# Kernel optimization log

Measured on AMD Instinct MI355X. Metric: run time of the kernel, lower is better.

Reference implementation:

```python
import jax, jax.numpy as jnp
import numpy as np

N = 100000
E = 1600000
IN_C, HID_C, OUT_C, NUM_CLASSES = 128, 64, 64, 40


def glorot(key, shape):
    lim = float(np.sqrt(6.0 / (shape[0] + shape[1])))
    return jax.random.uniform(key, shape, jnp.float32, -lim, lim)


def setup_inputs() -> dict:
    key = jax.random.key(0)
    ks = jax.random.split(key, 8)
    x = jax.random.normal(ks[0], (N, IN_C), jnp.float32)
    edge_index = jax.random.randint(ks[1], (2, E), 0, N, jnp.int64)
    return {
        "x": x,
        "edge_index": edge_index,
        "W1": glorot(ks[2], (IN_C, HID_C)),
        "b1": jnp.zeros((HID_C,), jnp.float32),
        "W2": glorot(ks[3], (HID_C, OUT_C)),
        "b2": jnp.zeros((OUT_C,), jnp.float32),
        "Wf": glorot(ks[4], (OUT_C, NUM_CLASSES)),
        "bf": jnp.zeros((NUM_CLASSES,), jnp.float32),
    }


def gcn_conv(x, W, b, src, dst, n):
    # PyG GCNConv: out = D^{-1/2} (A + I) D^{-1/2} (x W) + b, self-loops added.
    h = x @ W  # [N, C_out]
    loop = jnp.arange(n, dtype=src.dtype)
    src_f = jnp.concatenate([src, loop])  # [E+N]
    dst_f = jnp.concatenate([dst, loop])
    deg = jax.ops.segment_sum(jnp.ones_like(dst_f, dtype=h.dtype), dst_f,
                              num_segments=n)  # in-degree incl. self-loop
    inv_sqrt = jnp.where(deg > 0, jax.lax.rsqrt(deg), 0.0)
    norm = inv_sqrt[src_f] * inv_sqrt[dst_f]  # [E+N]
    msg = h[src_f] * norm[:, None]  # gather + scale, [E+N, C_out]
    out = jax.ops.segment_sum(msg, dst_f, num_segments=n)  # scatter-add
    return out + b


def reference(x, edge_index, W1, b1, W2, b2, Wf, bf):
    src, dst = edge_index[0], edge_index[1]
    n = x.shape[0]
    h = jax.nn.relu(gcn_conv(x, W1, b1, src, dst, n))
    h = jax.nn.relu(gcn_conv(h, W2, b2, src, dst, n))
    return h @ Wf + bf
```

## Files before the change

kernel.cpp:

```cpp
#include <hip/hip_runtime.h>

constexpr int N_NODES = 100000;
constexpr int N_EDGES = 1600000;
constexpr int IN_C  = 128;
constexpr int HID_C = 64;
constexpr int NUM_CLASSES = 40;

constexpr int BSH = 9;
constexpr int BUCK_N = 1 << BSH;
constexpr int NBUCK = (N_NODES + BUCK_N - 1) >> BSH;
constexpr int BCAP = 9216;
constexpr int FS_EPT = 16;
constexpr int FS_T = 256;
constexpr int FS_CHUNK = FS_EPT * FS_T;
constexpr int FS_BLKS = (N_EDGES + FS_CHUNK - 1) / FS_CHUNK;

typedef __attribute__((ext_vector_type(8))) short bf16x8;
typedef __attribute__((ext_vector_type(4))) short short4v;
typedef __attribute__((ext_vector_type(4))) float f32x4;

__device__ __forceinline__ unsigned short f2bf(float f) {
    unsigned u = __float_as_uint(f);
    return (unsigned short)((u + 0x7FFFu + ((u >> 16) & 1u)) >> 16);
}
__device__ __forceinline__ float bf2f(unsigned short h) {
    return __uint_as_float((unsigned)h << 16);
}

__global__ __launch_bounds__(FS_T) void fill_stage_kernel(
        const int* __restrict__ src, const int* __restrict__ dst,
        unsigned* __restrict__ gcur, unsigned* __restrict__ stage) {
    __shared__ unsigned hist[NBUCK];
    __shared__ unsigned rbase[NBUCK];
    int t = threadIdx.x;
    for (int i = t; i < NBUCK; i += FS_T) hist[i] = 0u;
    __syncthreads();
    int e0 = blockIdx.x * FS_CHUNK + t;
    unsigned pay[FS_EPT];
    unsigned br[FS_EPT];
#pragma unroll
    for (int i = 0; i < FS_EPT; ++i) {
        int e = e0 + i * FS_T;
        br[i] = 0xFFFFFFFFu; pay[i] = 0u;
        if (e < N_EDGES) {
            unsigned d = (unsigned)dst[e];
            unsigned s = (unsigned)src[e];
            unsigned b = d >> BSH;
            unsigned r = atomicAdd(&hist[b], 1u);
            pay[i] = (s << BSH) | (d & (BUCK_N - 1u));
            br[i]  = (b << 16) | r;
        }
    }
    __syncthreads();
    for (int i = t; i < NBUCK; i += FS_T) {
        unsigned c = hist[i];
        rbase[i] = c ? ((unsigned)i * BCAP + atomicAdd(&gcur[i], c)) : 0u;
    }
    __syncthreads();
#pragma unroll
    for (int i = 0; i < FS_EPT; ++i) {
        if (br[i] != 0xFFFFFFFFu) {
            unsigned bb = br[i] >> 16;
            unsigned idx = rbase[bb] + (br[i] & 0xFFFFu);
            if (idx < (bb + 1u) * BCAP) stage[idx] = pay[i];
        }
    }
}

__global__ __launch_bounds__(512) void fill_final_kernel(
        const unsigned* __restrict__ gcur,
        const unsigned* __restrict__ stage, unsigned* __restrict__ rowptr,
        float* __restrict__ inv, unsigned* __restrict__ csr_src) {
    __shared__ unsigned cur[BUCK_N];
    __shared__ unsigned ps[512];
    __shared__ unsigned buf[BCAP];
    int b = blockIdx.x, t = threadIdx.x;
    int lo = b << BSH;
    int nn = min(BUCK_N, N_NODES - lo);
    unsigned gv = (t < NBUCK) ? gcur[t] : 0u;
    ps[t] = gv;
    __syncthreads();
    for (int off = 1; off < 256; off <<= 1) {
        unsigned u = (t >= off) ? ps[t - off] : 0u;
        __syncthreads();
        ps[t] += u;
        __syncthreads();
    }
    unsigned base = ps[b] - gcur[b];
    if (b == NBUCK - 1 && t == 0) rowptr[N_NODES] = ps[NBUCK - 1];
    unsigned c = min(gcur[b], (unsigned)BCAP);
    const unsigned* st = stage + (size_t)b * BCAP;
    cur[t] = 0u;
    __syncthreads();
    for (int i = t; i < (int)c; i += 512) atomicAdd(&cur[st[i] & (BUCK_N - 1u)], 1u);
    __syncthreads();
    unsigned d = cur[t];
    ps[t] = d;
    __syncthreads();
    for (int off = 1; off < 512; off <<= 1) {
        unsigned u = (t >= off) ? ps[t - off] : 0u;
        __syncthreads();
        ps[t] += u;
        __syncthreads();
    }
    unsigned off0 = ps[t] - d;
    if (t < nn) {
        rowptr[lo + t] = base + off0;
        inv[lo + t] = rsqrtf((float)(d + 1u));
    }
    __syncthreads();
    cur[t] = off0;
    __syncthreads();
    for (int i = t; i < (int)c; i += 512) {
        unsigned v = st[i];
        unsigned pos = atomicAdd(&cur[v & (BUCK_N - 1u)], 1u);
        buf[pos] = v >> BSH;
    }
    __syncthreads();
    for (int i = t; i < (int)c; i += 512) csr_src[base + i] = buf[i];
}

template <int K, bool BF>
__global__ __launch_bounds__(256) void gemm_mfma_kernel(
        const void* __restrict__ Xv, const float* __restrict__ W,
        const float* __restrict__ inv, unsigned short* __restrict__ out, int n) {
    __shared__ __align__(16) short Asd[64][K + 8];
    __shared__ __align__(16) short Bsd[64][K + 8];
    int t = threadIdx.x;
    int n0 = blockIdx.x * 64;
    if (BF) {
        const uint4* Xb = (const uint4*)Xv;
        for (int i = t; i < 64 * (K / 8); i += 256) {
            int row = i / (K / 8), seg = i % (K / 8);
            int node = n0 + row;
            uint4 v = {0, 0, 0, 0};
            if (node < n) v = Xb[(size_t)node * (K / 8) + seg];
            *(uint4*)&Asd[row][seg * 8] = v;
        }
    } else {
        const float* Xf = (const float*)Xv;
        for (int i = t; i < 64 * (K / 4); i += 256) {
            int row = i / (K / 4), seg = i % (K / 4);
            int node = n0 + row;
            float4 v = {0, 0, 0, 0};
            if (node < n) v = *(const float4*)&Xf[(size_t)node * K + seg * 4];
            short4v o;
            o.x = (short)f2bf(v.x); o.y = (short)f2bf(v.y);
            o.z = (short)f2bf(v.z); o.w = (short)f2bf(v.w);
            *(short4v*)&Asd[row][seg * 4] = o;
        }
    }
    for (int i = t; i < K * 16; i += 256) {
        int k = i >> 4, ng = i & 15;
        float4 v = *(const float4*)&W[(size_t)k * 64 + ng * 4];
        Bsd[ng * 4 + 0][k] = (short)f2bf(v.x);
        Bsd[ng * 4 + 1][k] = (short)f2bf(v.y);
        Bsd[ng * 4 + 2][k] = (short)f2bf(v.z);
        Bsd[ng * 4 + 3][k] = (short)f2bf(v.w);
    }
    __syncthreads();
    int wv = t >> 6, lane = t & 63;
    int m = lane & 15, quad = lane >> 4;
    int rowbase = wv * 16;
    f32x4 acc0 = {0,0,0,0}, acc1 = {0,0,0,0}, acc2 = {0,0,0,0}, acc3 = {0,0,0,0};
#pragma unroll
    for (int kb = 0; kb < K / 32; ++kb) {
        bf16x8 af = *(const bf16x8*)&Asd[rowbase + m][kb * 32 + quad * 8];
        bf16x8 b0 = *(const bf16x8*)&Bsd[ 0 + m][kb * 32 + quad * 8];
        bf16x8 b1 = *(const bf16x8*)&Bsd[16 + m][kb * 32 + quad * 8];
        bf16x8 b2 = *(const bf16x8*)&Bsd[32 + m][kb * 32 + quad * 8];
        bf16x8 b3 = *(const bf16x8*)&Bsd[48 + m][kb * 32 + quad * 8];
        acc0 = __builtin_amdgcn_mfma_f32_16x16x32_bf16(af, b0, acc0, 0, 0, 0);
        acc1 = __builtin_amdgcn_mfma_f32_16x16x32_bf16(af, b1, acc1, 0, 0, 0);
        acc2 = __builtin_amdgcn_mfma_f32_16x16x32_bf16(af, b2, acc2, 0, 0, 0);
        acc3 = __builtin_amdgcn_mfma_f32_16x16x32_bf16(af, b3, acc3, 0, 0, 0);
    }
    f32x4 accs[4] = {acc0, acc1, acc2, acc3};
#pragma unroll
    for (int r = 0; r < 4; ++r) {
        int node = n0 + rowbase + quad * 4 + r;
        if (node < n) {
            float sc = inv[node];
#pragma unroll
            for (int s = 0; s < 4; ++s)
                out[(size_t)node * 64 + s * 16 + m] = f2bf(accs[s][r] * sc);
        }
    }
}

__global__ __launch_bounds__(256) void agg_fused_kernel(
        const unsigned* __restrict__ rowptr, const unsigned* __restrict__ csr_src,
        const unsigned short* __restrict__ hs, const float* __restrict__ inv,
        const float* __restrict__ bias, unsigned short* __restrict__ out) {
    int t = threadIdx.x;
    int lane = t & 63;
    int oct = lane >> 3;
    int cl  = lane & 7;
    int node = blockIdx.x * 32 + (t >> 6) * 8 + oct;
    unsigned beg = rowptr[node], end = rowptr[node + 1];
    float a0 = 0.f, a1 = 0.f, a2 = 0.f, a3 = 0.f;
    float a4 = 0.f, a5 = 0.f, a6 = 0.f, a7 = 0.f;
    const uint4* hsrow = (const uint4*)hs;
#pragma unroll 4
    for (unsigned e = beg; e < end; ++e) {
        unsigned s = csr_src[e];
        uint4 v = hsrow[(size_t)s * 8 + cl];
        a0 += __uint_as_float(v.x << 16);
        a1 += __uint_as_float(v.x & 0xFFFF0000u);
        a2 += __uint_as_float(v.y << 16);
        a3 += __uint_as_float(v.y & 0xFFFF0000u);
        a4 += __uint_as_float(v.z << 16);
        a5 += __uint_as_float(v.z & 0xFFFF0000u);
        a6 += __uint_as_float(v.w << 16);
        a7 += __uint_as_float(v.w & 0xFFFF0000u);
    }
    uint4 sv = hsrow[(size_t)node * 8 + cl];
    float4 bv0 = *(const float4*)&bias[cl * 8];
    float4 bv1 = *(const float4*)&bias[cl * 8 + 4];
    float s = inv[node];
    float r0 = fmaxf(s * (a0 + __uint_as_float(sv.x << 16))         + bv0.x, 0.f);
    float r1 = fmaxf(s * (a1 + __uint_as_float(sv.x & 0xFFFF0000u)) + bv0.y, 0.f);
    float r2 = fmaxf(s * (a2 + __uint_as_float(sv.y << 16))         + bv0.z, 0.f);
    float r3 = fmaxf(s * (a3 + __uint_as_float(sv.y & 0xFFFF0000u)) + bv0.w, 0.f);
    float r4 = fmaxf(s * (a4 + __uint_as_float(sv.z << 16))         + bv1.x, 0.f);
    float r5 = fmaxf(s * (a5 + __uint_as_float(sv.z & 0xFFFF0000u)) + bv1.y, 0.f);
    float r6 = fmaxf(s * (a6 + __uint_as_float(sv.w << 16))         + bv1.z, 0.f);
    float r7 = fmaxf(s * (a7 + __uint_as_float(sv.w & 0xFFFF0000u)) + bv1.w, 0.f);
    uint4 o;
    o.x = (unsigned)f2bf(r0) | ((unsigned)f2bf(r1) << 16);
    o.y = (unsigned)f2bf(r2) | ((unsigned)f2bf(r3) << 16);
    o.z = (unsigned)f2bf(r4) | ((unsigned)f2bf(r5) << 16);
    o.w = (unsigned)f2bf(r6) | ((unsigned)f2bf(r7) << 16);
    ((uint4*)out)[(size_t)node * 8 + cl] = o;
}

__global__ __launch_bounds__(320) void final_gemm_kernel(
        const unsigned short* __restrict__ H, const float* __restrict__ Wf,
        const float* __restrict__ bfv, float* __restrict__ out, int n) {
    constexpr int CK = 64, J = 40;
    __shared__ float Ws[CK * J];
    __shared__ float Hs[CK][132];
    int t = threadIdx.x;
    int n0 = blockIdx.x * 128;
    for (int i = t; i < CK * J / 4; i += 320)
        ((float4*)Ws)[i] = ((const float4*)Wf)[i];
    for (int i = t; i < 128 * 16; i += 320) {
        int row = i >> 4, kc = i & 15;
        int node = n0 + row;
        ushort4 v = {0, 0, 0, 0};
        if (node < n) v = *(const ushort4*)&H[(size_t)node * 64 + kc * 4];
        Hs[kc * 4 + 0][row] = bf2f(v.x);
        Hs[kc * 4 + 1][row] = bf2f(v.y);
        Hs[kc * 4 + 2][row] = bf2f(v.z);
        Hs[kc * 4 + 3][row] = bf2f(v.w);
    }
    __syncthreads();
    int cg = t % 10;
    int rg = t / 10;
    float4 a0 = {0,0,0,0}, a1 = {0,0,0,0}, a2 = {0,0,0,0}, a3 = {0,0,0,0};
#pragma unroll 8
    for (int k = 0; k < CK; ++k) {
        float4 b = *(const float4*)&Ws[k * J + cg * 4];
        float4 a = *(const float4*)&Hs[k][rg * 4];
        a0.x += a.x * b.x; a0.y += a.x * b.y; a0.z += a.x * b.z; a0.w += a.x * b.w;
        a1.x += a.y * b.x; a1.y += a.y * b.y; a1.z += a.y * b.z; a1.w += a.y * b.w;
        a2.x += a.z * b.x; a2.y += a.z * b.y; a2.z += a.z * b.z; a2.w += a.z * b.w;
        a3.x += a.w * b.x; a3.y += a.w * b.y; a3.z += a.w * b.z; a3.w += a.w * b.w;
    }
    float4 bv = *(const float4*)&bfv[cg * 4];
    float4 accs[4] = {a0, a1, a2, a3};
#pragma unroll
    for (int i = 0; i < 4; ++i) {
        int node = n0 + rg * 4 + i;
        if (node < n) {
            float4 r = accs[i];
            r.x += bv.x; r.y += bv.y; r.z += bv.z; r.w += bv.w;
            *(float4*)&out[(size_t)node * J + cg * 4] = r;
        }
    }
}

extern "C" void kernel_launch(void* const* d_in, const int* in_sizes, int n_in,
                              void* d_out, int out_size, void* d_ws, size_t ws_size,
                              hipStream_t stream) {
    const float* x  = (const float*)d_in[0];
    const int*   ei = (const int*)d_in[1];
    const float* W1 = (const float*)d_in[2];
    const float* b1 = (const float*)d_in[3];
    const float* W2 = (const float*)d_in[4];
    const float* b2 = (const float*)d_in[5];
    const float* Wf = (const float*)d_in[6];
    const float* bf = (const float*)d_in[7];
    float* out = (float*)d_out;

    const int* src = ei;
    const int* dst = ei + N_EDGES;

    char* ws = (char*)d_ws;
    unsigned* rowptr  = (unsigned*)(ws + 0);
    float*    inv     = (float*)   (ws + 400064);
    unsigned* gcur    = (unsigned*)(ws + 800064);
    unsigned* csr_src = (unsigned*)(ws + 801792);
    unsigned short* A = (unsigned short*)(ws + 7201792);
    unsigned short* B = (unsigned short*)(ws + 20001792);
    unsigned* stage   = (unsigned*)A;

    hipMemsetAsync(gcur, 0, NBUCK * sizeof(unsigned), stream);
    fill_stage_kernel<<<FS_BLKS, FS_T, 0, stream>>>(src, dst, gcur, stage);
    fill_final_kernel<<<NBUCK, 512, 0, stream>>>(gcur, stage, rowptr, inv, csr_src);

    gemm_mfma_kernel<IN_C, false>
        <<<(N_NODES + 63) / 64, 256, 0, stream>>>(x, W1, inv, A, N_NODES);
    agg_fused_kernel<<<N_NODES / 32, 256, 0, stream>>>(rowptr, csr_src, A, inv, b1, B);

    gemm_mfma_kernel<HID_C, true>
        <<<(N_NODES + 63) / 64, 256, 0, stream>>>(B, W2, inv, A, N_NODES);
    agg_fused_kernel<<<N_NODES / 32, 256, 0, stream>>>(rowptr, csr_src, A, inv, b2, B);

    final_gemm_kernel<<<(N_NODES + 127) / 128, 320, 0, stream>>>(B, Wf, bf, out, N_NODES);
}
```

Baseline: 244.8 us.

## Fuse aggregation with following GEMM to drop intermediate feature round-trips

Layer-1 aggregation is merged with the layer-2 MFMA GEMM, and layer-2 aggregation is merged with the final classifier GEMM. Each block aggregates 64 nodes into shared memory, then multiplies by the weights directly. This removes two kernel launches and the global write and re-read of the bf16 hidden activations. In exchange, the latency-bound gather phase now shares a block with GEMM work. The final GEMM also uses only 160 of 256 threads, which could lower occupancy or overlap.

```diff
diff --git a/kernel.cpp b/kernel.cpp
--- a/kernel.cpp
+++ b/kernel.cpp
@@ -120,87 +120,12 @@
     for (int i = t; i < (int)c; i += 512) csr_src[base + i] = buf[i];
 }
 
-template <int K, bool BF>
-__global__ __launch_bounds__(256) void gemm_mfma_kernel(
-        const void* __restrict__ Xv, const float* __restrict__ W,
-        const float* __restrict__ inv, unsigned short* __restrict__ out, int n) {
-    __shared__ __align__(16) short Asd[64][K + 8];
-    __shared__ __align__(16) short Bsd[64][K + 8];
-    int t = threadIdx.x;
-    int n0 = blockIdx.x * 64;
-    if (BF) {
-        const uint4* Xb = (const uint4*)Xv;
-        for (int i = t; i < 64 * (K / 8); i += 256) {
-            int row = i / (K / 8), seg = i % (K / 8);
-            int node = n0 + row;
-            uint4 v = {0, 0, 0, 0};
-            if (node < n) v = Xb[(size_t)node * (K / 8) + seg];
-            *(uint4*)&Asd[row][seg * 8] = v;
-        }
-    } else {
-        const float* Xf = (const float*)Xv;
-        for (int i = t; i < 64 * (K / 4); i += 256) {
-            int row = i / (K / 4), seg = i % (K / 4);
-            int node = n0 + row;
-            float4 v = {0, 0, 0, 0};
-            if (node < n) v = *(const float4*)&Xf[(size_t)node * K + seg * 4];
-            short4v o;
-            o.x = (short)f2bf(v.x); o.y = (short)f2bf(v.y);
-            o.z = (short)f2bf(v.z); o.w = (short)f2bf(v.w);
-            *(short4v*)&Asd[row][seg * 4] = o;
-        }
-    }
-    for (int i = t; i < K * 16; i += 256) {
-        int k = i >> 4, ng = i & 15;
-        float4 v = *(const float4*)&W[(size_t)k * 64 + ng * 4];
-        Bsd[ng * 4 + 0][k] = (short)f2bf(v.x);
-        Bsd[ng * 4 + 1][k] = (short)f2bf(v.y);
-        Bsd[ng * 4 + 2][k] = (short)f2bf(v.z);
-        Bsd[ng * 4 + 3][k] = (short)f2bf(v.w);
-    }
-    __syncthreads();
-    int wv = t >> 6, lane = t & 63;
-    int m = lane & 15, quad = lane >> 4;
-    int rowbase = wv * 16;
-    f32x4 acc0 = {0,0,0,0}, acc1 = {0,0,0,0}, acc2 = {0,0,0,0}, acc3 = {0,0,0,0};
-#pragma unroll
-    for (int kb = 0; kb < K / 32; ++kb) {
-        bf16x8 af = *(const bf16x8*)&Asd[rowbase + m][kb * 32 + quad * 8];
-        bf16x8 b0 = *(const bf16x8*)&Bsd[ 0 + m][kb * 32 + quad * 8];
-        bf16x8 b1 = *(const bf16x8*)&Bsd[16 + m][kb * 32 + quad * 8];
-        bf16x8 b2 = *(const bf16x8*)&Bsd[32 + m][kb * 32 + quad * 8];
-        bf16x8 b3 = *(const bf16x8*)&Bsd[48 + m][kb * 32 + quad * 8];
-        acc0 = __builtin_amdgcn_mfma_f32_16x16x32_bf16(af, b0, acc0, 0, 0, 0);
-        acc1 = __builtin_amdgcn_mfma_f32_16x16x32_bf16(af, b1, acc1, 0, 0, 0);
-        acc2 = __builtin_amdgcn_mfma_f32_16x16x32_bf16(af, b2, acc2, 0, 0, 0);
-        acc3 = __builtin_amdgcn_mfma_f32_16x16x32_bf16(af, b3, acc3, 0, 0, 0);
-    }
-    f32x4 accs[4] = {acc0, acc1, acc2, acc3};
-#pragma unroll
-    for (int r = 0; r < 4; ++r) {
-        int node = n0 + rowbase + quad * 4 + r;
-        if (node < n) {
-            float sc = inv[node];
-#pragma unroll
-            for (int s = 0; s < 4; ++s)
-                out[(size_t)node * 64 + s * 16 + m] = f2bf(accs[s][r] * sc);
-        }
-    }
-}
-
-__global__ __launch_bounds__(256) void agg_fused_kernel(
+__device__ __forceinline__ void agg_sums(
         const unsigned* __restrict__ rowptr, const unsigned* __restrict__ csr_src,
-        const unsigned short* __restrict__ hs, const float* __restrict__ inv,
-        const float* __restrict__ bias, unsigned short* __restrict__ out) {
-    int t = threadIdx.x;
-    int lane = t & 63;
-    int oct = lane >> 3;
-    int cl  = lane & 7;
-    int node = blockIdx.x * 32 + (t >> 6) * 8 + oct;
+        const uint4* __restrict__ hsrow, int node, int cl,
+        float& a0, float& a1, float& a2, float& a3,
+        float& a4, float& a5, float& a6, float& a7) {
     unsigned beg = rowptr[node], end = rowptr[node + 1];
-    float a0 = 0.f, a1 = 0.f, a2 = 0.f, a3 = 0.f;
-    float a4 = 0.f, a5 = 0.f, a6 = 0.f, a7 = 0.f;
-    const uint4* hsrow = (const uint4*)hs;
 #pragma unroll 4
     for (unsigned e = beg; e < end; ++e) {
         unsigned s = csr_src[e];
@@ -214,68 +139,215 @@
         a6 += __uint_as_float(v.w << 16);
         a7 += __uint_as_float(v.w & 0xFFFF0000u);
     }
-    uint4 sv = hsrow[(size_t)node * 8 + cl];
+}
+
+__global__ __launch_bounds__(256) void gemm_mfma_kernel(
+        const float* __restrict__ Xf, const float* __restrict__ W,
+        const float* __restrict__ inv, unsigned short* __restrict__ out, int n) {
+    constexpr int K = IN_C;
+    __shared__ __align__(16) short Asd[64][K + 8];
+    __shared__ __align__(16) short Bsd[64][K + 8];
+    int t = threadIdx.x;
+    int n0 = blockIdx.x * 64;
+    for (int i = t; i < 64 * (K / 4); i += 256) {
+        int row = i / (K / 4), seg = i % (K / 4);
+        int node = n0 + row;
+        float4 v = {0, 0, 0, 0};
+        if (node < n) v = *(const float4*)&Xf[(size_t)node * K + seg * 4];
+        short4v o;
+        o.x = (short)f2bf(v.x); o.y = (short)f2bf(v.y);
+        o.z = (short)f2bf(v.z); o.w = (short)f2bf(v.w);
+        *(short4v*)&Asd[row][seg * 4] = o;
+    }
+    for (int i = t; i < K * 16; i += 256) {
+        int k = i >> 4, ng = i & 15;
+        float4 v = *(const float4*)&W[(size_t)k * 64 + ng * 4];
+        Bsd[ng * 4 + 0][k] = (short)f2bf(v.x);
+        Bsd[ng * 4 + 1][k] = (short)f2bf(v.y);
+        Bsd[ng * 4 + 2][k] = (short)f2bf(v.z);
+        Bsd[ng * 4 + 3][k] = (short)f2bf(v.w);
+    }
+    __syncthreads();
+    int wv = t >> 6, lane = t & 63;
+    int m = lane & 15, quad = lane >> 4;
+    int rowbase = wv * 16;
+    f32x4 acc0 = {0,0,0,0}, acc1 = {0,0,0,0}, acc2 = {0,0,0,0}, acc3 = {0,0,0,0};
+#pragma unroll
+    for (int kb = 0; kb < K / 32; ++kb) {
+        bf16x8 af = *(const bf16x8*)&Asd[rowbase + m][kb * 32 + quad * 8];
+        bf16x8 b0 = *(const bf16x8*)&Bsd[ 0 + m][kb * 32 + quad * 8];
+        bf16x8 b1 = *(const bf16x8*)&Bsd[16 + m][kb * 32 + quad * 8];
+        bf16x8 b2 = *(const bf16x8*)&Bsd[32 + m][kb * 32 + quad * 8];
+        bf16x8 b3 = *(const bf16x8*)&Bsd[48 + m][kb * 32 + quad * 8];
+        acc0 = __builtin_amdgcn_mfma_f32_16x16x32_bf16(af, b0, acc0, 0, 0, 0);
+        acc1 = __builtin_amdgcn_mfma_f32_16x16x32_bf16(af, b1, acc1, 0, 0, 0);
+        acc2 = __builtin_amdgcn_mfma_f32_16x16x32_bf16(af, b2, acc2, 0, 0, 0);
+        acc3 = __builtin_amdgcn_mfma_f32_16x16x32_bf16(af, b3, acc3, 0, 0, 0);
+    }
+    f32x4 accs[4] = {acc0, acc1, acc2, acc3};
+#pragma unroll
+    for (int r = 0; r < 4; ++r) {
+        int node = n0 + rowbase + quad * 4 + r;
+        if (node < n) {
+            float sc = inv[node];
+#pragma unroll
+            for (int s = 0; s < 4; ++s)
+                out[(size_t)node * 64 + s * 16 + m] = f2bf(accs[s][r] * sc);
+        }
+    }
+}
+
+__global__ __launch_bounds__(256) void agg_gemm2_kernel(
+        const unsigned* __restrict__ rowptr, const unsigned* __restrict__ csr_src,
+        const unsigned short* __restrict__ hs, const float* __restrict__ inv,
+        const float* __restrict__ bias, const float* __restrict__ W,
+        unsigned short* __restrict__ out, int n) {
+    constexpr int K = HID_C;
+    __shared__ __align__(16) short Asd[64][K + 8];
+    __shared__ __align__(16) short Bsd[64][K + 8];
+    int t = threadIdx.x;
+    int n0 = blockIdx.x * 64;
+    int lane = t & 63, wv = t >> 6;
+    int oct = lane >> 3, cl = lane & 7;
+    const uint4* hsrow = (const uint4*)hs;
+    for (int i = t; i < K * 16; i += 256) {
+        int k = i >> 4, ng = i & 15;
+        float4 v = *(const float4*)&W[(size_t)k * 64 + ng * 4];
+        Bsd[ng * 4 + 0][k] = (short)f2bf(v.x);
+        Bsd[ng * 4 + 1][k] = (short)f2bf(v.y);
+        Bsd[ng * 4 + 2][k] = (short)f2bf(v.z);
+        Bsd[ng * 4 + 3][k] = (short)f2bf(v.w);
+    }
     float4 bv0 = *(const float4*)&bias[cl * 8];
     float4 bv1 = *(const float4*)&bias[cl * 8 + 4];
-    float s = inv[node];
-    float r0 = fmaxf(s * (a0 + __uint_as_float(sv.x << 16))         + bv0.x, 0.f);
-    float r1 = fmaxf(s * (a1 + __uint_as_float(sv.x & 0xFFFF0000u)) + bv0.y, 0.f);
-    float r2 = fmaxf(s * (a2 + __uint_as_float(sv.y << 16))         + bv0.z, 0.f);
-    float r3 = fmaxf(s * (a3 + __uint_as_float(sv.y & 0xFFFF0000u)) + bv0.w, 0.f);
-    float r4 = fmaxf(s * (a4 + __uint_as_float(sv.z << 16))         + bv1.x, 0.f);
-    float r5 = fmaxf(s * (a5 + __uint_as_float(sv.z & 0xFFFF0000u)) + bv1.y, 0.f);
-    float r6 = fmaxf(s * (a6 + __uint_as_float(sv.w << 16))         + bv1.z, 0.f);
-    float r7 = fmaxf(s * (a7 + __uint_as_float(sv.w & 0xFFFF0000u)) + bv1.w, 0.f);
-    uint4 o;
-    o.x = (unsigned)f2bf(r0) | ((unsigned)f2bf(r1) << 16);
-    o.y = (unsigned)f2bf(r2) | ((unsigned)f2bf(r3) << 16);
-    o.z = (unsigned)f2bf(r4) | ((unsigned)f2bf(r5) << 16);
-    o.w = (unsigned)f2bf(r6) | ((unsigned)f2bf(r7) << 16);
-    ((uint4*)out)[(size_t)node * 8 + cl] = o;
-}
-
-__global__ __launch_bounds__(320) void final_gemm_kernel(
-        const unsigned short* __restrict__ H, const float* __restrict__ Wf,
+#pragma unroll
+    for (int p = 0; p < 2; ++p) {
+        int nl = p * 32 + wv * 8 + oct;
+        int node = n0 + nl;
+        float r0 = 0.f, r1 = 0.f, r2 = 0.f, r3 = 0.f;
+        float r4 = 0.f, r5 = 0.f, r6 = 0.f, r7 = 0.f;
+        if (node < n) {
+            float a0 = 0.f, a1 = 0.f, a2 = 0.f, a3 = 0.f;
+            float a4 = 0.f, a5 = 0.f, a6 = 0.f, a7 = 0.f;
+            agg_sums(rowptr, csr_src, hsrow, node, cl, a0, a1, a2, a3, a4, a5, a6, a7);
+            uint4 sv = hsrow[(size_t)node * 8 + cl];
+            float s = inv[node];
+            r0 = fmaxf(s * (a0 + __uint_as_float(sv.x << 16))         + bv0.x, 0.f);
+            r1 = fmaxf(s * (a1 + __uint_as_float(sv.x & 0xFFFF0000u)) + bv0.y, 0.f);
+            r2 = fmaxf(s * (a2 + __uint_as_float(sv.y << 16))         + bv0.z, 0.f);
+            r3 = fmaxf(s * (a3 + __uint_as_float(sv.y & 0xFFFF0000u)) + bv0.w, 0.f);
+            r4 = fmaxf(s * (a4 + __uint_as_float(sv.z << 16))         + bv1.x, 0.f);
+            r5 = fmaxf(s * (a5 + __uint_as_float(sv.z & 0xFFFF0000u)) + bv1.y, 0.f);
+            r6 = fmaxf(s * (a6 + __uint_as_float(sv.w << 16))         + bv1.z, 0.f);
+            r7 = fmaxf(s * (a7 + __uint_as_float(sv.w & 0xFFFF0000u)) + bv1.w, 0.f);
+        }
+        uint4 o;
+        o.x = (unsigned)f2bf(r0) | ((unsigned)f2bf(r1) << 16);
+        o.y = (unsigned)f2bf(r2) | ((unsigned)f2bf(r3) << 16);
+        o.z = (unsigned)f2bf(r4) | ((unsigned)f2bf(r5) << 16);
+        o.w = (unsigned)f2bf(r6) | ((unsigned)f2bf(r7) << 16);
+        *(uint4*)&Asd[nl][cl * 8] = o;
+    }
+    __syncthreads();
+    int m = lane & 15, quad = lane >> 4;
+    int rowbase = wv * 16;
+    f32x4 acc0 = {0,0,0,0}, acc1 = {0,0,0,0}, acc2 = {0,0,0,0}, acc3 = {0,0,0,0};
+#pragma unroll
+    for (int kb = 0; kb < K / 32; ++kb) {
+        bf16x8 af = *(const bf16x8*)&Asd[rowbase + m][kb * 32 + quad * 8];
+        bf16x8 b0 = *(const bf16x8*)&Bsd[ 0 + m][kb * 32 + quad * 8];
+        bf16x8 b1 = *(const bf16x8*)&Bsd[16 + m][kb * 32 + quad * 8];
+        bf16x8 b2 = *(const bf16x8*)&Bsd[32 + m][kb * 32 + quad * 8];
+        bf16x8 b3 = *(const bf16x8*)&Bsd[48 + m][kb * 32 + quad * 8];
+        acc0 = __builtin_amdgcn_mfma_f32_16x16x32_bf16(af, b0, acc0, 0, 0, 0);
+        acc1 = __builtin_amdgcn_mfma_f32_16x16x32_bf16(af, b1, acc1, 0, 0, 0);
+        acc2 = __builtin_amdgcn_mfma_f32_16x16x32_bf16(af, b2, acc2, 0, 0, 0);
+        acc3 = __builtin_amdgcn_mfma_f32_16x16x32_bf16(af, b3, acc3, 0, 0, 0);
+    }
+    f32x4 accs[4] = {acc0, acc1, acc2, acc3};
+#pragma unroll
+    for (int r = 0; r < 4; ++r) {
+        int node = n0 + rowbase + quad * 4 + r;
+        if (node < n) {
+            float sc = inv[node];
+#pragma unroll
+            for (int s = 0; s < 4; ++s)
+                out[(size_t)node * 64 + s * 16 + m] = f2bf(accs[s][r] * sc);
+        }
+    }
+}
+
+__global__ __launch_bounds__(256) void agg_final_kernel(
+        const unsigned* __restrict__ rowptr, const unsigned* __restrict__ csr_src,
+        const unsigned short* __restrict__ hs, const float* __restrict__ inv,
+        const float* __restrict__ bias, const float* __restrict__ Wf,
         const float* __restrict__ bfv, float* __restrict__ out, int n) {
     constexpr int CK = 64, J = 40;
     __shared__ float Ws[CK * J];
-    __shared__ float Hs[CK][132];
+    __shared__ float Hs[CK][68];
     int t = threadIdx.x;
-    int n0 = blockIdx.x * 128;
-    for (int i = t; i < CK * J / 4; i += 320)
+    int n0 = blockIdx.x * 64;
+    int lane = t & 63, wv = t >> 6;
+    int oct = lane >> 3, cl = lane & 7;
+    const uint4* hsrow = (const uint4*)hs;
+    for (int i = t; i < CK * J / 4; i += 256)
         ((float4*)Ws)[i] = ((const float4*)Wf)[i];
-    for (int i = t; i < 128 * 16; i += 320) {
-        int row = i >> 4, kc = i & 15;
-        int node = n0 + row;
-        ushort4 v = {0, 0, 0, 0};
-        if (node < n) v = *(const ushort4*)&H[(size_t)node * 64 + kc * 4];
-        Hs[kc * 4 + 0][row] = bf2f(v.x);
-        Hs[kc * 4 + 1][row] = bf2f(v.y);
-        Hs[kc * 4 + 2][row] = bf2f(v.z);
-        Hs[kc * 4 + 3][row] = bf2f(v.w);
-    }
-    __syncthreads();
-    int cg = t % 10;
-    int rg = t / 10;
-    float4 a0 = {0,0,0,0}, a1 = {0,0,0,0}, a2 = {0,0,0,0}, a3 = {0,0,0,0};
+    float4 bv0 = *(const float4*)&bias[cl * 8];
+    float4 bv1 = *(const float4*)&bias[cl * 8 + 4];
+#pragma unroll
+    for (int p = 0; p < 2; ++p) {
+        int nl = p * 32 + wv * 8 + oct;
+        int node = n0 + nl;
+        float r0 = 0.f, r1 = 0.f, r2 = 0.f, r3 = 0.f;
+        float r4 = 0.f, r5 = 0.f, r6 = 0.f, r7 = 0.f;
+        if (node < n) {
+            float a0 = 0.f, a1 = 0.f, a2 = 0.f, a3 = 0.f;
+            float a4 = 0.f, a5 = 0.f, a6 = 0.f, a7 = 0.f;
+            agg_sums(rowptr, csr_src, hsrow, node, cl, a0, a1, a2, a3, a4, a5, a6, a7);
+            uint4 sv = hsrow[(size_t)node * 8 + cl];
+            float s = inv[node];
+            r0 = fmaxf(s * (a0 + __uint_as_float(sv.x << 16))         + bv0.x, 0.f);
+            r1 = fmaxf(s * (a1 + __uint_as_float(sv.x & 0xFFFF0000u)) + bv0.y, 0.f);
+            r2 = fmaxf(s * (a2 + __uint_as_float(sv.y << 16))         + bv0.z, 0.f);
+            r3 = fmaxf(s * (a3 + __uint_as_float(sv.y & 0xFFFF0000u)) + bv0.w, 0.f);
+            r4 = fmaxf(s * (a4 + __uint_as_float(sv.z << 16))         + bv1.x, 0.f);
+            r5 = fmaxf(s * (a5 + __uint_as_float(sv.z & 0xFFFF0000u)) + bv1.y, 0.f);
+            r6 = fmaxf(s * (a6 + __uint_as_float(sv.w << 16))         + bv1.z, 0.f);
+            r7 = fmaxf(s * (a7 + __uint_as_float(sv.w & 0xFFFF0000u)) + bv1.w, 0.f);
+        }
+        Hs[cl * 8 + 0][nl] = r0;
+        Hs[cl * 8 + 1][nl] = r1;
+        Hs[cl * 8 + 2][nl] = r2;
+        Hs[cl * 8 + 3][nl] = r3;
+        Hs[cl * 8 + 4][nl] = r4;
+        Hs[cl * 8 + 5][nl] = r5;
+        Hs[cl * 8 + 6][nl] = r6;
+        Hs[cl * 8 + 7][nl] = r7;
+    }
+    __syncthreads();
+    if (t < 160) {
+        int cg = t % 10;
+        int rg = t / 10;
+        float4 a0 = {0,0,0,0}, a1 = {0,0,0,0}, a2 = {0,0,0,0}, a3 = {0,0,0,0};
 #pragma unroll 8
-    for (int k = 0; k < CK; ++k) {
-        float4 b = *(const float4*)&Ws[k * J + cg * 4];
-        float4 a = *(const float4*)&Hs[k][rg * 4];
-        a0.x += a.x * b.x; a0.y += a.x * b.y; a0.z += a.x * b.z; a0.w += a.x * b.w;
-        a1.x += a.y * b.x; a1.y += a.y * b.y; a1.z += a.y * b.z; a1.w += a.y * b.w;
-        a2.x += a.z * b.x; a2.y += a.z * b.y; a2.z += a.z * b.z; a2.w += a.z * b.w;
-        a3.x += a.w * b.x; a3.y += a.w * b.y; a3.z += a.w * b.z; a3.w += a.w * b.w;
-    }
-    float4 bv = *(const float4*)&bfv[cg * 4];
-    float4 accs[4] = {a0, a1, a2, a3};
-#pragma unroll
-    for (int i = 0; i < 4; ++i) {
-        int node = n0 + rg * 4 + i;
-        if (node < n) {
-            float4 r = accs[i];
-            r.x += bv.x; r.y += bv.y; r.z += bv.z; r.w += bv.w;
-            *(float4*)&out[(size_t)node * J + cg * 4] = r;
+        for (int k = 0; k < CK; ++k) {
+            float4 b = *(const float4*)&Ws[k * J + cg * 4];
+            float4 a = *(const float4*)&Hs[k][rg * 4];
+            a0.x += a.x * b.x; a0.y += a.x * b.y; a0.z += a.x * b.z; a0.w += a.x * b.w;
+            a1.x += a.y * b.x; a1.y += a.y * b.y; a1.z += a.y * b.z; a1.w += a.y * b.w;
+            a2.x += a.z * b.x; a2.y += a.z * b.y; a2.z += a.z * b.z; a2.w += a.z * b.w;
+            a3.x += a.w * b.x; a3.y += a.w * b.y; a3.z += a.w * b.z; a3.w += a.w * b.w;
+        }
+        float4 bv = *(const float4*)&bfv[cg * 4];
+        float4 accs[4] = {a0, a1, a2, a3};
+#pragma unroll
+        for (int i = 0; i < 4; ++i) {
+            int node = n0 + rg * 4 + i;
+            if (node < n) {
+                float4 r = accs[i];
+                r.x += bv.x; r.y += bv.y; r.z += bv.z; r.w += bv.w;
+                *(float4*)&out[(size_t)node * J + cg * 4] = r;
+            }
         }
     }
 }
@@ -309,13 +381,11 @@
     fill_stage_kernel<<<FS_BLKS, FS_T, 0, stream>>>(src, dst, gcur, stage);
     fill_final_kernel<<<NBUCK, 512, 0, stream>>>(gcur, stage, rowptr, inv, csr_src);
 
-    gemm_mfma_kernel<IN_C, false>
-        <<<(N_NODES + 63) / 64, 256, 0, stream>>>(x, W1, inv, A, N_NODES);
-    agg_fused_kernel<<<N_NODES / 32, 256, 0, stream>>>(rowptr, csr_src, A, inv, b1, B);
-
-    gemm_mfma_kernel<HID_C, true>
-        <<<(N_NODES + 63) / 64, 256, 0, stream>>>(B, W2, inv, A, N_NODES);
-    agg_fused_kernel<<<N_NODES / 32, 256, 0, stream>>>(rowptr, csr_src, A, inv, b2, B);
-
-    final_gemm_kernel<<<(N_NODES + 127) / 128, 320, 0, stream>>>(B, Wf, bf, out, N_NODES);
-}
+    gemm_mfma_kernel<<<(N_NODES + 63) / 64, 256, 0, stream>>>(x, W1, inv, A, N_NODES);
+
+    agg_gemm2_kernel<<<(N_NODES + 63) / 64, 256, 0, stream>>>(
+        rowptr, csr_src, A, inv, b1, W2, B, N_NODES);
+
+    agg_final_kernel<<<(N_NODES + 63) / 64, 256, 0, stream>>>(
+        rowptr, csr_src, B, inv, b2, Wf, bf, out, N_NODES);
+}
```

Result: faster. 236.8 us (-3.3%).
